# Optimization experiments

Hardware: AMD Instinct MI355X
Metric: run time of the kernel (lower is better)

## Reference

```python
import jax, jax.numpy as jnp
import numpy as np
from jax import lax


def ternarize(w):
    """Standard TWN ternarization with straight-through estimator.
    delta = 0.7*mean(|w|); alpha = mean(|w|) over kept entries; w_t = alpha*sign(w)*mask.
    """
    a = jnp.abs(w)
    delta = 0.7 * a.mean()
    mask = (a > delta).astype(w.dtype)
    alpha = (a * mask).sum() / jnp.maximum(mask.sum(), 1.0)
    wt = alpha * jnp.sign(w) * mask
    return w + lax.stop_gradient(wt - w)  # STE


def conv3x3(x, w, b):
    y = lax.conv_general_dilated(x, ternarize(w), window_strides=(1, 1),
                                 padding=((1, 1), (1, 1)),
                                 dimension_numbers=('NCHW', 'OIHW', 'NCHW'))
    return y + b[None, :, None, None]


def maxpool2(x):
    return lax.reduce_window(x, -jnp.inf, lax.max, (1, 1, 2, 2), (1, 1, 2, 2), 'VALID')


def setup_inputs() -> dict:
    key = jax.random.key(0)
    ks = jax.random.split(key, 11)
    s = lambda k, shape, scale: jax.random.normal(k, shape, dtype=jnp.float32) * scale
    return {
        'x':   s(ks[0], (1024, 3, 32, 32), 1.0),
        'w1':  s(ks[1], (64, 3, 3, 3), 0.1),
        'b1':  s(ks[2], (64,), 0.01),
        'w2':  s(ks[3], (128, 64, 3, 3), 0.05),
        'b2':  s(ks[4], (128,), 0.01),
        'w3':  s(ks[5], (256, 128, 3, 3), 0.03),
        'b3':  s(ks[6], (256,), 0.01),
        'wf1': s(ks[7], (256, 4096), 0.02),
        'bf1': s(ks[8], (256,), 0.01),
        'wf2': s(ks[9], (10, 256), 0.06),
        'bf2': s(ks[10], (10,), 0.01),
    }


def reference(x, w1, b1, w2, b2, w3, b3, wf1, bf1, wf2, bf2):
    x = maxpool2(jax.nn.relu(conv3x3(x, w1, b1)))   # [B,64,16,16]
    x = maxpool2(jax.nn.relu(conv3x3(x, w2, b2)))   # [B,128,8,8]
    x = maxpool2(jax.nn.relu(conv3x3(x, w3, b3)))   # [B,256,4,4]
    x = x.reshape(-1, 256 * 4 * 4)
    x = jax.nn.relu(x @ ternarize(wf1).T + bf1)     # [B,256]
    return x @ ternarize(wf2).T + bf2               # [B,10]
```

## Files before the change

kernel.cpp:

```cpp
#include <hip/hip_runtime.h>
#include <hip/hip_bf16.h>


typedef __attribute__((ext_vector_type(8))) short short8;
typedef __attribute__((ext_vector_type(4))) float f32x4;
typedef __attribute__((ext_vector_type(4))) int i32x4;

#define GLOAD_LDS16(g, l)                                              \
    __builtin_amdgcn_global_load_lds(                                  \
        (const __attribute__((address_space(1))) void*)(g),            \
        (__attribute__((address_space(3))) void*)(l), 16, 0, 0)

__device__ __forceinline__ unsigned short f2bf(float x) {
    unsigned u = __float_as_uint(x);
    return (unsigned short)((u + 0x7fffu + ((u >> 16) & 1u)) >> 16);
}
__device__ __forceinline__ float bf2f(unsigned short b) {
    return __uint_as_float(((unsigned)b) << 16);
}

#define WS_W1B   0
#define N_W1B    2048
#define WS_W2P   (WS_W1B + N_W1B)
#define N_W2P    (9*128*64)
#define WS_W3P   (WS_W2P + N_W2P)
#define N_W3P    (9*256*128)
#define WS_WTF1  (WS_W3P + N_W3P)
#define N_WTF1   (256*4096)
#define WS_WTF2  (WS_WTF1 + N_WTF1)
#define N_WTF2   (10*256)
#define WS_A1    (WS_WTF2 + N_WTF2)
#define N_A1     (1024*256*64)
#define WS_A2    (WS_A1 + N_A1)
#define N_A2     (1024*64*128)
#define WS_A3    (WS_A2 + N_A2)
#define N_A3     (1024*16*256)
#define WS_F1    (WS_A3 + N_A3)
#define N_F1     (1024*256)
#define WS_SCR   (WS_F1 + N_F1)

#define FC1_S    16

struct TernArgs {
    const float* w[6];
    int n[6];
};

__global__ void tern_stats1(TernArgs ta, double* __restrict__ scr) {
    const int wi = blockIdx.y;
    const float* __restrict__ w = ta.w[wi];
    const int n = ta.n[wi];
    __shared__ double red[4];
    const int lane = threadIdx.x & 63, wv = threadIdx.x >> 6;
    if (wi == 5) {
        float m = 0.f;
        for (int i = blockIdx.x * blockDim.x + threadIdx.x; i < n;
             i += gridDim.x * blockDim.x)
            m = fmaxf(m, fabsf(w[i]));
        #pragma unroll
        for (int off = 32; off > 0; off >>= 1)
            m = fmaxf(m, __shfl_down(m, off, 64));
        if (lane == 0) red[wv] = (double)m;
        __syncthreads();
        if (threadIdx.x == 0) {
            float mm = (float)fmax(fmax(red[0], red[1]), fmax(red[2], red[3]));
            atomicMax((int*)(scr + 20), __float_as_int(mm));
        }
        return;
    }
    double s = 0.0;
    for (int i = blockIdx.x * blockDim.x + threadIdx.x; i < n;
         i += gridDim.x * blockDim.x)
        s += (double)fabsf(w[i]);
    #pragma unroll
    for (int off = 32; off > 0; off >>= 1) s += __shfl_down(s, off, 64);
    if (lane == 0) red[wv] = s;
    __syncthreads();
    if (threadIdx.x == 0)
        atomicAdd(scr + wi * 4, red[0] + red[1] + red[2] + red[3]);
}

__global__ void tern_stats2(TernArgs ta, double* __restrict__ scr) {
    const int wi = blockIdx.y;
    const float* __restrict__ w = ta.w[wi];
    const int n = ta.n[wi];
    const float delta = (float)(0.7 * scr[wi * 4] / (double)n);
    double ms = 0.0, cnt = 0.0;
    for (int i = blockIdx.x * blockDim.x + threadIdx.x; i < n;
         i += gridDim.x * blockDim.x) {
        float a = fabsf(w[i]);
        if (a > delta) { ms += (double)a; cnt += 1.0; }
    }
    #pragma unroll
    for (int off = 32; off > 0; off >>= 1) {
        ms += __shfl_down(ms, off, 64);
        cnt += __shfl_down(cnt, off, 64);
    }
    __shared__ double redm[4], redc[4];
    const int lane = threadIdx.x & 63, wv = threadIdx.x >> 6;
    if (lane == 0) { redm[wv] = ms; redc[wv] = cnt; }
    __syncthreads();
    if (threadIdx.x == 0) {
        atomicAdd(scr + wi * 4 + 1, redm[0] + redm[1] + redm[2] + redm[3]);
        atomicAdd(scr + wi * 4 + 2, redc[0] + redc[1] + redc[2] + redc[3]);
    }
}

__global__ void tern_write_all(TernArgs ta, const double* __restrict__ scr,
                               signed char* __restrict__ w1b,
                               signed char* __restrict__ w2p8,
                               signed char* __restrict__ w3p8,
                               unsigned short* __restrict__ wtf1b,
                               float* __restrict__ wtf2) {
    const int wi = blockIdx.y;
    const float* __restrict__ w = ta.w[wi];
    const int n = ta.n[wi];
    const double* sc = scr + wi * 4;
    const float delta = (float)(0.7 * sc[0] / (double)n);
    const int i0 = blockIdx.x * blockDim.x + threadIdx.x;
    const int stride = gridDim.x * blockDim.x;

    if (wi == 0) {
        for (int i = i0; i < n; i += stride) {
            const int co = i / 27;
            const int kp = i % 27;
            float v = w[i];
            signed char s = (fabsf(v) > delta) ? (v > 0.0f ? 1 : -1) : 0;
            w1b[co * 64 + kp] = s;
            w1b[4096 + co * 64 + 32 + kp] = s;
        }
    } else if (wi == 4) {
        const double c = sc[2];
        const float alpha = (float)(sc[1] / (c > 1.0 ? c : 1.0));
        for (int i = i0; i < n; i += stride) {
            float v = w[i];
            wtf2[i] = (fabsf(v) > delta) ? (v > 0.0f ? alpha : -alpha) : 0.0f;
        }
    } else if (wi == 1 || wi == 2) {
        const int CIc = (wi == 1) ? 64 : 128;
        const int COc = (wi == 1) ? 128 : 256;
        signed char* dst = (wi == 1) ? w2p8 : w3p8;
        for (int i = i0; i < n; i += stride) {
            const int co = i / (CIc * 9);
            const int r = i % (CIc * 9);
            const int ci = r / 9, tap = r % 9;
            float v = w[i];
            signed char s = (fabsf(v) > delta) ? (v > 0.0f ? 1 : -1) : 0;
            dst[(tap * COc + co) * CIc + ci] = s;
        }
    } else {
        for (int i = i0; i < n; i += stride) {
            const int j = i >> 12;
            const int k = i & 4095;
            const int c = k >> 4, px = k & 15;
            float v = w[i];
            unsigned short s = (fabsf(v) > delta) ? (v > 0.0f ? 0x3f80 : 0xbf80) : 0;
            unsigned short* row = wtf1b + ((long)j << 13) + px * 512 + c;
            row[0] = s;
            row[256] = s;
        }
    }
}

__global__ __launch_bounds__(256) void conv1_i8(
        const float* __restrict__ x,
        const signed char* __restrict__ w1b,
        const float* __restrict__ bias,
        const double* __restrict__ scr,
        const int* __restrict__ amax_x,
        int* __restrict__ amax_out,
        float* __restrict__ y) {
    constexpr int PL = 3472;
    __shared__ __align__(16) char X[2 * PL];
    __shared__ float redm[4];

    const int b = blockIdx.x;
    const int tid = threadIdx.x;
    const float S = 32512.0f / fmaxf(__int_as_float(*amax_x), 1e-30f);

    for (int i = tid; i < 2 * PL / 16; i += 256)
        ((int4*)X)[i] = make_int4(0, 0, 0, 0);
    __syncthreads();

    for (int i = tid; i < 768; i += 256) {
        const float4 v = ((const float4*)(x + (long)b * 3072))[i];
        const int e = i * 4;
        const int ci = e >> 10;
        const int rem = e & 1023;
        const int h = rem >> 5, w = rem & 31;
        const int base = ci * 1156 + (h + 1) * 34 + (w + 1);
        const float f[4] = {v.x, v.y, v.z, v.w};
        #pragma unroll
        for (int j = 0; j < 4; j++) {
            const int q = __float2int_rn(f[j] * S);
            const int ql = (q << 24) >> 24;
            const int qh = (q - ql) >> 8;
            X[base + j] = (char)ql;
            X[PL + base + j] = (char)qh;
        }
    }
    __syncthreads();

    const int lane = tid & 63;
    const int wid = tid >> 6;
    const int lm = lane & 15;
    const int kg = lane >> 4;

    const int poff = (kg >= 2) ? PL : 0;
    int cst[16];
    #pragma unroll
    for (int j = 0; j < 16; j++) {
        const int kp = (kg & 1) * 16 + j;
        cst[j] = (kp < 27)
                     ? ((kp / 9) * 1156 + ((kp % 9) / 3) * 34 + (kp % 9) % 3)
                     : 0;
    }

    i32x4 BL[4], BH[4];
    #pragma unroll
    for (int nt = 0; nt < 4; nt++) {
        const int co = nt * 16 + lm;
        BL[nt] = *(const i32x4*)(w1b + (long)co * 64 + kg * 16);
        BH[nt] = *(const i32x4*)(w1b + 4096 + (long)co * 64 + kg * 16);
    }

    const double c2 = scr[2];
    const float alpha = (float)(scr[1] / (c2 > 1.0 ? c2 : 1.0));
    const float dq = alpha / S;
    float tmax = 0.f;
    float* yb = y + (long)b * 256 * 64;

    for (int tt = 0; tt < 16; ++tt) {
        const int t = wid * 16 + tt;
        const int pp = t * 4 + (lm >> 2);
        const int sub = lm & 3;
        const int h = 2 * (pp >> 4) + (sub >> 1);
        const int w = 2 * (pp & 15) + (sub & 1);
        const int base = poff + h * 34 + w;
        unsigned d[4] = {0u, 0u, 0u, 0u};
        #pragma unroll
        for (int j = 0; j < 16; j++) {
            const unsigned byte = (unsigned char)X[base + cst[j]];
            d[j >> 2] |= byte << ((j & 3) * 8);
        }
        i32x4 Af;
        Af[0] = (int)d[0]; Af[1] = (int)d[1];
        Af[2] = (int)d[2]; Af[3] = (int)d[3];

        const int opp = t * 4 + kg;
        float* yr = yb + (long)opp * 64;
        #pragma unroll
        for (int nt = 0; nt < 4; nt++) {
            i32x4 aL = 0, aH = 0;
            aL = __builtin_amdgcn_mfma_i32_16x16x64_i8(Af, BL[nt], aL, 0, 0, 0);
            aH = __builtin_amdgcn_mfma_i32_16x16x64_i8(Af, BH[nt], aH, 0, 0, 0);
            const int s0 = aH[0] * 256 + aL[0];
            const int s1 = aH[1] * 256 + aL[1];
            const int s2 = aH[2] * 256 + aL[2];
            const int s3 = aH[3] * 256 + aL[3];
            int sm = s0 > s1 ? s0 : s1;
            const int sn = s2 > s3 ? s2 : s3;
            sm = sm > sn ? sm : sn;
            const int co = nt * 16 + lm;
            const float o = fmaxf(dq * (float)sm + bias[co], 0.f);
            tmax = fmaxf(tmax, o);
            yr[co] = o;
        }
    }

    #pragma unroll
    for (int off = 32; off > 0; off >>= 1)
        tmax = fmaxf(tmax, __shfl_down(tmax, off, 64));
    if (lane == 0) redm[wid] = tmax;
    __syncthreads();
    if (tid == 0) {
        float m = fmaxf(fmaxf(redm[0], redm[1]), fmaxf(redm[2], redm[3]));
        atomicMax(amax_out, __float_as_int(m));
    }
}

template <int CI, int HI, int CO, int HB, int WM, int WN, bool INF32>
__global__ __launch_bounds__(256, 2) void conv_i8(
        const void* __restrict__ xin,
        const signed char* __restrict__ wp,
        const float* __restrict__ bias,
        const double* __restrict__ scr,
        const int* __restrict__ amax_in,
        int* __restrict__ amax_out,
        unsigned short* __restrict__ yout) {
    constexpr int CH8 = CI / 64;
    constexpr int NITER = 9 * CH8;
    constexpr int HR = HI / HB;
    constexpr int ROWS = HR + 2;
    constexpr int COLS = HI + 2;
    constexpr int NPIX = ROWS * COLS;
    constexpr int PSTR = NPIX * 64 + 32;
    constexpr int PO = HI / 2;
    constexpr int POR = HR / 2;
    constexpr int MT = 4, NT = 4;
    constexpr int RWB = HI * CI * 4;
    constexpr int RAWR = (HB == 1) ? (ROWS - 2) : (ROWS - 1);
    static_assert(WM * WN == 4, "4 waves");
    static_assert(WM * 64 == HR * HI, "M covers slab pixels");
    static_assert(WN * 64 == CO, "N covers all co");
    static_assert(RWB == 4096, "row must be 4096 B");
    static_assert(HB <= 2, "row compaction assumes <=1 invalid row per end");
    static_assert((COLS & 1) == 0, "swizzle parity uses even COLS");

    __shared__ __align__(16) char X[2 * CH8 * PSTR];
    __shared__ __align__(16) char RAW[RAWR * RWB];
    __shared__ float redm[4];

    const int bimg = blockIdx.x / HB;
    const int hb = blockIdx.x % HB;
    const int tid = threadIdx.x;
    const int lane = tid & 63;
    const int wid = tid >> 6;

    const float S = 32512.0f / fmaxf(__int_as_float(*amax_in), 1e-30f);

    const int rlo = (hb == 0) ? 1 : 0;
    const int rhi = (hb == HB - 1) ? (ROWS - 1) : ROWS;
    for (int r = rlo; r < rhi; r++) {
        if (wid == (r & 3)) {
            const int h = hb * HR + r - 1;
            const int rl = r - rlo;
            const char* grow = (const char*)xin +
                               ((long)(bimg * HI + h)) * RWB;
            #pragma unroll
            for (int j = 0; j < RWB / 1024; j++)
                GLOAD_LDS16(grow + j * 1024 + lane * 16,
                            &RAW[rl * RWB + j * 1024]);
        }
    }

    constexpr int HALO = 2 * COLS + 2 * (ROWS - 2);
    for (int i = tid; i < HALO * 2 * CH8 * 4; i += 256) {
        const int u = i & 3;
        const int t = i >> 2;
        const int g = t % (2 * CH8);
        const int hp = t / (2 * CH8);
        int p;
        if (hp < COLS) p = hp;
        else if (hp < 2 * COLS) p = (ROWS - 1) * COLS + (hp - COLS);
        else {
            const int e = hp - 2 * COLS;
            p = (1 + (e >> 1)) * COLS + ((e & 1) ? (COLS - 1) : 0);
        }
        *(int4*)&X[g * PSTR + p * 64 + u * 16] = make_int4(0, 0, 0, 0);
    }
    __syncthreads();

    if (INF32) {
        constexpr int NIT = RAWR * HI * (CI / 4);
        for (int i = tid; i < NIT; i += 256) {
            const int q4 = i % (CI / 4);
            const int t = i / (CI / 4);
            const int c = t % HI;
            const int rl = t / HI;
            const int r = rlo + rl;
            const float4 v =
                *(const float4*)&RAW[rl * RWB + c * (CI * 4) + q4 * 16];
            const float f[4] = {v.x, v.y, v.z, v.w};
            unsigned pl = 0, ph = 0;
            #pragma unroll
            for (int j = 0; j < 4; j++) {
                const int qi = (int)(f[j] * S + 0.5f);
                pl |= (unsigned)(qi & 255) << (j * 8);
                ph |= (unsigned)(((qi + 128) >> 8) & 255) << (j * 8);
            }
            const int p = r * COLS + c + 1;
            const int cc = (q4 * 4) & 63;
            const int ch = q4 / 16;
            const int slot = ((cc >> 4) + ((c + 1) >> 1) + 2 * r) & 3;
            const int base = p * 64 + slot * 16 + (cc & 15);
            *(unsigned*)&X[ch * PSTR + base] = pl;
            *(unsigned*)&X[(CH8 + ch) * PSTR + base] = ph;
        }
    } else {
        constexpr int NIT = RAWR * HI * (CI / 8);
        for (int i = tid; i < NIT; i += 256) {
            const int q8 = i % (CI / 8);
            const int t = i / (CI / 8);
            const int c = t % HI;
            const int rl = t / HI;
            const int r = rlo + rl;
            const uint4 vh =
                *(const uint4*)&RAW[rl * RWB + c * (CI * 4) + q8 * 16];
            const uint4 vl =
                *(const uint4*)&RAW[rl * RWB + c * (CI * 4) + CI * 2 +
                                    q8 * 16];
            const unsigned* hw = (const unsigned*)&vh;
            const unsigned* lw = (const unsigned*)&vl;
            float f[8];
            #pragma unroll
            for (int j = 0; j < 8; j++) {
                const unsigned hu = (j & 1) ? (hw[j >> 1] >> 16)
                                            : (hw[j >> 1] & 0xffffu);
                const unsigned lu = (j & 1) ? (lw[j >> 1] >> 16)
                                            : (lw[j >> 1] & 0xffffu);
                f[j] = __uint_as_float(hu << 16) + __uint_as_float(lu << 16);
            }
            unsigned pl0 = 0, pl1 = 0, ph0 = 0, ph1 = 0;
            #pragma unroll
            for (int j = 0; j < 8; j++) {
                const int qi = (int)(f[j] * S + 0.5f);
                const int sh = (j & 3) * 8;
                const unsigned lb = (unsigned)(qi & 255) << sh;
                const unsigned hbyte =
                    (unsigned)(((qi + 128) >> 8) & 255) << sh;
                if (j < 4) { pl0 |= lb; ph0 |= hbyte; }
                else       { pl1 |= lb; ph1 |= hbyte; }
            }
            const int p = r * COLS + c + 1;
            const int ch = q8 / 8;
            const int cc = (q8 * 8) & 63;
            const int slot = ((cc >> 4) + ((c + 1) >> 1) + 2 * r) & 3;
            const int base = p * 64 + slot * 16 + (cc & 15);
            *(uint2*)&X[ch * PSTR + base] = make_uint2(pl0, pl1);
            *(uint2*)&X[(CH8 + ch) * PSTR + base] = make_uint2(ph0, ph1);
        }
    }
    __syncthreads();

    const int wm = (WM == 1) ? 0 : (wid >> 1);
    const int wn = (WM == 1) ? wid : (wid & 1);
    const int lm = lane & 15;
    const int kg = lane >> 4;

    int pq[MT];
    #pragma unroll
    for (int mt = 0; mt < MT; mt++) {
        const int m = (wm * MT + mt) * 16 + lm;
        const int pp = m >> 2, sub = m & 3;
        const int lph = pp / PO, lpw = pp % PO;
        const int h = 2 * lph + (sub >> 1);
        const int w = 2 * lpw + (sub & 1);
        pq[mt] = ((h * COLS + w) << 6) | ((h & 1) << 3) | (w & 7);
    }
    const signed char* bp[NT];
    #pragma unroll
    for (int nt = 0; nt < NT; nt++) {
        const int co = (wn * NT + nt) * 16 + lm;
        bp[nt] = wp + (long)co * CI + kg * 16;
    }

    i32x4 accL[MT][NT], accH[MT][NT];
    #pragma unroll
    for (int mt = 0; mt < MT; mt++)
        #pragma unroll
        for (int nt = 0; nt < NT; nt++) { accL[mt][nt] = 0; accH[mt][nt] = 0; }

    i32x4 Bb[2][NT];
    #pragma unroll
    for (int nt = 0; nt < NT; nt++) Bb[0][nt] = *(const i32x4*)(bp[nt]);

    #pragma unroll 2
    for (int it = 0; it < NITER; ++it) {
        const int cur = it & 1, nxt = cur ^ 1;
        if (it + 1 < NITER) {
            const int it1 = it + 1;
            const int tap = it1 / CH8, ch1 = it1 % CH8;
            const int woff = tap * CO * CI + ch1 * 64;
            #pragma unroll
            for (int nt = 0; nt < NT; nt++)
                Bb[nxt][nt] = *(const i32x4*)(bp[nt] + woff);
        }
        const int tap = it / CH8, ch = it % CH8;
        const int ty = tap / 3, tx = tap % 3;
        const int DT = (ty * COLS + tx) << 6;
        const int typ = ty & 1;
        int ao[MT];
        #pragma unroll
        for (int mt = 0; mt < MT; mt++) {
            const int q = pq[mt];
            const int slot = (kg + ((((q >> 3) & 1) + typ) & 1) * 2 +
                              (((q & 7) + tx) >> 1)) & 3;
            ao[mt] = (q & ~63) + DT + (slot << 4);
        }
        {
            i32x4 Af[MT];
            #pragma unroll
            for (int mt = 0; mt < MT; mt++)
                Af[mt] = *(const i32x4*)&X[ch * PSTR + ao[mt]];
            #pragma unroll
            for (int mt = 0; mt < MT; mt++)
                #pragma unroll
                for (int nt = 0; nt < NT; nt++)
                    accL[mt][nt] = __builtin_amdgcn_mfma_i32_16x16x64_i8(
                        Af[mt], Bb[cur][nt], accL[mt][nt], 0, 0, 0);
        }
        {
            i32x4 Af[MT];
            #pragma unroll
            for (int mt = 0; mt < MT; mt++)
                Af[mt] = *(const i32x4*)&X[(CH8 + ch) * PSTR + ao[mt]];
            #pragma unroll
            for (int mt = 0; mt < MT; mt++)
                #pragma unroll
                for (int nt = 0; nt < NT; nt++)
                    accH[mt][nt] = __builtin_amdgcn_mfma_i32_16x16x64_i8(
                        Af[mt], Bb[cur][nt], accH[mt][nt], 0, 0, 0);
        }
    }

    const double c2 = scr[2];
    const float alpha = (float)(scr[1] / (c2 > 1.0 ? c2 : 1.0));
    const float dq = alpha / S;
    float tmax = 0.f;
    #pragma unroll
    for (int mt = 0; mt < MT; mt++) {
        const int pp = (wm * MT + mt) * 4 + kg;
        const int lph = pp / PO, lpw = pp % PO;
        const int gpp = (hb * POR + lph) * PO + lpw;
        unsigned short* yr = yout + ((long)bimg * (PO * PO) + gpp) * (2 * CO);
        #pragma unroll
        for (int nt = 0; nt < NT; nt++) {
            const int co = (wn * NT + nt) * 16 + lm;
            const i32x4 aL = accL[mt][nt], aH = accH[mt][nt];
            int s0 = aH[0] * 256 + aL[0];
            int s1 = aH[1] * 256 + aL[1];
            int s2 = aH[2] * 256 + aL[2];
            int s3 = aH[3] * 256 + aL[3];
            int sm = s0 > s1 ? s0 : s1;
            int sn = s2 > s3 ? s2 : s3;
            sm = sm > sn ? sm : sn;
            float o = fmaxf(dq * (float)sm + bias[co], 0.f);
            tmax = fmaxf(tmax, o);
            unsigned short hi = f2bf(o);
            unsigned short lo = f2bf(o - bf2f(hi));
            yr[co] = hi;
            yr[CO + co] = lo;
        }
    }
    if (amax_out) {
        #pragma unroll
        for (int off = 32; off > 0; off >>= 1)
            tmax = fmaxf(tmax, __shfl_down(tmax, off, 64));
        if (lane == 0) redm[wid] = tmax;
        __syncthreads();
        if (tid == 0) {
            float m = fmaxf(fmaxf(redm[0], redm[1]), fmaxf(redm[2], redm[3]));
            atomicMax(amax_out, __float_as_int(m));
        }
    }
}

template <int S>
__global__ __launch_bounds__(256) void fc1_mfma(
        const unsigned short* __restrict__ A,
        const unsigned short* __restrict__ Bw,
        float* __restrict__ parts) {
    constexpr int KCH = 8192 / S;
    constexpr int NSTEP = KCH / 32;
    const int m0 = blockIdx.x * 128;
    const int n0 = blockIdx.y * 128;
    const int s = blockIdx.z;
    const int tid = threadIdx.x;
    const int lane = tid & 63, wid = tid >> 6;
    const int wm = wid >> 1, wn = wid & 1;
    const int lm = lane & 15, kg = lane >> 4;

    const long k0 = (long)s * KCH + kg * 8;
    const unsigned short* ap[4];
    const unsigned short* bp[4];
    #pragma unroll
    for (int t = 0; t < 4; t++) {
        ap[t] = A + (long)(m0 + wm * 64 + t * 16 + lm) * 8192 + k0;
        bp[t] = Bw + (long)(n0 + wn * 64 + t * 16 + lm) * 8192 + k0;
    }

    f32x4 acc[4][4] = {};
    short8 Ab[2][4], Bb[2][4];
    #pragma unroll
    for (int t = 0; t < 4; t++) {
        Ab[0][t] = *(const short8*)(ap[t]);
        Bb[0][t] = *(const short8*)(bp[t]);
    }

    #pragma unroll 2
    for (int st = 0; st < NSTEP; ++st) {
        const int cur = st & 1, nxt = cur ^ 1;
        if (st + 1 < NSTEP) {
            const int off = (st + 1) * 32;
            #pragma unroll
            for (int t = 0; t < 4; t++) {
                Ab[nxt][t] = *(const short8*)(ap[t] + off);
                Bb[nxt][t] = *(const short8*)(bp[t] + off);
            }
        }
        #pragma unroll
        for (int mt = 0; mt < 4; mt++)
            #pragma unroll
            for (int nt = 0; nt < 4; nt++)
                acc[mt][nt] = __builtin_amdgcn_mfma_f32_16x16x32_bf16(
                    Ab[cur][mt], Bb[cur][nt], acc[mt][nt], 0, 0, 0);
    }

    #pragma unroll
    for (int mt = 0; mt < 4; mt++) {
        #pragma unroll
        for (int r = 0; r < 4; r++) {
            const int b = m0 + wm * 64 + mt * 16 + kg * 4 + r;
            #pragma unroll
            for (int nt = 0; nt < 4; nt++) {
                const int j = n0 + wn * 64 + nt * 16 + lm;
                parts[((long)s * 1024 + b) * 256 + j] = acc[mt][nt][r];
            }
        }
    }
}

template <int S>
__global__ __launch_bounds__(256) void fc2_fused(
        const float* __restrict__ parts,
        const double* __restrict__ scr,
        const float* __restrict__ bf1v,
        const float* __restrict__ wtf2,
        const float* __restrict__ bf2v,
        float* __restrict__ out) {
    __shared__ float sf[256];
    const int b = blockIdx.x;
    const int j = threadIdx.x;
    float s = 0.f;
    #pragma unroll
    for (int p = 0; p < S; p++)
        s += parts[(long)p * 262144 + (long)b * 256 + j];
    const double c2 = scr[2];
    const float alpha = (float)(scr[1] / (c2 > 1.0 ? c2 : 1.0));
    sf[j] = fmaxf(alpha * s + bf1v[j], 0.f);
    __syncthreads();
    const int lane = threadIdx.x & 63, wid = threadIdx.x >> 6;
    for (int k = wid; k < 10; k += 4) {
        const float* wr = wtf2 + k * 256;
        float acc = 0.f;
        #pragma unroll
        for (int t = 0; t < 4; t++)
            acc += sf[lane + t * 64] * wr[lane + t * 64];
        #pragma unroll
        for (int off = 32; off > 0; off >>= 1)
            acc += __shfl_down(acc, off, 64);
        if (lane == 0) out[(long)b * 10 + k] = acc + bf2v[k];
    }
}

extern "C" void kernel_launch(void* const* d_in, const int* in_sizes, int n_in,
                              void* d_out, int out_size, void* d_ws, size_t ws_size,
                              hipStream_t stream) {
    const float* x   = (const float*)d_in[0];
    const float* w1  = (const float*)d_in[1];
    const float* b1  = (const float*)d_in[2];
    const float* w2  = (const float*)d_in[3];
    const float* b2  = (const float*)d_in[4];
    const float* w3  = (const float*)d_in[5];
    const float* b3  = (const float*)d_in[6];
    const float* wf1 = (const float*)d_in[7];
    const float* bf1 = (const float*)d_in[8];
    const float* wf2 = (const float*)d_in[9];
    const float* bf2 = (const float*)d_in[10];
    float* out = (float*)d_out;
    float* ws = (float*)d_ws;

    const int B = 1024;

    signed char*    w1b   = (signed char*)(ws + WS_W1B);
    signed char*    w2p8  = (signed char*)(ws + WS_W2P);
    signed char*    w3p8  = (signed char*)(ws + WS_W3P);
    unsigned short* wtf1b = (unsigned short*)(ws + WS_WTF1);
    float*          wtf2  = ws + WS_WTF2;
    float*          a1f   = ws + WS_A1;
    unsigned short* a2p   = (unsigned short*)(ws + WS_A2);
    unsigned short* a3p   = (unsigned short*)(ws + WS_A3);
    double*         scr   = (double*)(ws + WS_SCR);
    int*            iscr  = (int*)(scr + 20);
    int*            amaxx = iscr;
    int*            amax1 = iscr + 1;
    int*            amax2 = iscr + 2;
    float*          parts = ws + WS_A1;

    hipMemsetAsync(scr, 0, 22 * sizeof(double), stream);
    hipMemsetAsync(w1b, 0, 8192, stream);

    TernArgs ta;
    ta.w[0] = w1;  ta.n[0] = 64 * 27;
    ta.w[1] = w2;  ta.n[1] = 128 * 64 * 9;
    ta.w[2] = w3;  ta.n[2] = 256 * 128 * 9;
    ta.w[3] = wf1; ta.n[3] = 256 * 4096;
    ta.w[4] = wf2; ta.n[4] = 10 * 256;
    ta.w[5] = x;   ta.n[5] = 1024 * 3 * 32 * 32;

    hipLaunchKernelGGL(tern_stats1, dim3(128, 6), dim3(256), 0, stream, ta, scr);
    hipLaunchKernelGGL(tern_stats2, dim3(128, 5), dim3(256), 0, stream, ta, scr);
    hipLaunchKernelGGL(tern_write_all, dim3(128, 5), dim3(256), 0, stream,
                       ta, scr, w1b, w2p8, w3p8, wtf1b, wtf2);

    hipLaunchKernelGGL(conv1_i8, dim3(B), dim3(256), 0, stream,
                       x, w1b, b1, scr + 0, amaxx, amax1, a1f);

    hipLaunchKernelGGL((conv_i8<64, 16, 128, 2, 2, 2, true>), dim3(B * 2),
                       dim3(256), 0, stream, a1f, w2p8, b2, scr + 4, amax1,
                       amax2, a2p);

    hipLaunchKernelGGL((conv_i8<128, 8, 256, 1, 1, 4, false>), dim3(B),
                       dim3(256), 0, stream, a2p, w3p8, b3, scr + 8, amax2,
                       (int*)nullptr, a3p);

    hipLaunchKernelGGL((fc1_mfma<FC1_S>), dim3(8, 2, FC1_S), dim3(256), 0, stream,
                       a3p, wtf1b, parts);

    hipLaunchKernelGGL((fc2_fused<FC1_S>), dim3(B), dim3(256), 0, stream,
                       parts, scr + 12, bf1, wtf2, bf2, out);
}
```

Baseline: 280.6 us.

## Process multiple slabs per block and prefetch next slab during epilogue

The conv_i8 kernel becomes persistent over NSLAB slabs per block, halving the grid for conv2 and conv3. The next slab's raw rows are issued via global_load_lds before the current slab's epilogue stores, overlapping load latency with output writes, and bias is hoisted into registers. Halo zeroing runs only once, except for the bottom row, which is re-zeroed when slabs alternate. The trade is fewer blocks, so less parallelism and occupancy across CUs, in exchange for amortized setup and overlapped loads.

```diff
diff --git a/kernel.cpp b/kernel.cpp
--- a/kernel.cpp
+++ b/kernel.cpp
@@ -279,7 +279,7 @@
     }
 }
 
-template <int CI, int HI, int CO, int HB, int WM, int WN, bool INF32>
+template <int CI, int HI, int CO, int HB, int WM, int WN, bool INF32, int NSLAB>
 __global__ __launch_bounds__(256, 2) void conv_i8(
         const void* __restrict__ xin,
         const signed char* __restrict__ wp,
@@ -311,117 +311,14 @@
     __shared__ __align__(16) char RAW[RAWR * RWB];
     __shared__ float redm[4];
 
-    const int bimg = blockIdx.x / HB;
-    const int hb = blockIdx.x % HB;
     const int tid = threadIdx.x;
     const int lane = tid & 63;
     const int wid = tid >> 6;
 
     const float S = 32512.0f / fmaxf(__int_as_float(*amax_in), 1e-30f);
-
-    const int rlo = (hb == 0) ? 1 : 0;
-    const int rhi = (hb == HB - 1) ? (ROWS - 1) : ROWS;
-    for (int r = rlo; r < rhi; r++) {
-        if (wid == (r & 3)) {
-            const int h = hb * HR + r - 1;
-            const int rl = r - rlo;
-            const char* grow = (const char*)xin +
-                               ((long)(bimg * HI + h)) * RWB;
-            #pragma unroll
-            for (int j = 0; j < RWB / 1024; j++)
-                GLOAD_LDS16(grow + j * 1024 + lane * 16,
-                            &RAW[rl * RWB + j * 1024]);
-        }
-    }
-
-    constexpr int HALO = 2 * COLS + 2 * (ROWS - 2);
-    for (int i = tid; i < HALO * 2 * CH8 * 4; i += 256) {
-        const int u = i & 3;
-        const int t = i >> 2;
-        const int g = t % (2 * CH8);
-        const int hp = t / (2 * CH8);
-        int p;
-        if (hp < COLS) p = hp;
-        else if (hp < 2 * COLS) p = (ROWS - 1) * COLS + (hp - COLS);
-        else {
-            const int e = hp - 2 * COLS;
-            p = (1 + (e >> 1)) * COLS + ((e & 1) ? (COLS - 1) : 0);
-        }
-        *(int4*)&X[g * PSTR + p * 64 + u * 16] = make_int4(0, 0, 0, 0);
-    }
-    __syncthreads();
-
-    if (INF32) {
-        constexpr int NIT = RAWR * HI * (CI / 4);
-        for (int i = tid; i < NIT; i += 256) {
-            const int q4 = i % (CI / 4);
-            const int t = i / (CI / 4);
-            const int c = t % HI;
-            const int rl = t / HI;
-            const int r = rlo + rl;
-            const float4 v =
-                *(const float4*)&RAW[rl * RWB + c * (CI * 4) + q4 * 16];
-            const float f[4] = {v.x, v.y, v.z, v.w};
-            unsigned pl = 0, ph = 0;
-            #pragma unroll
-            for (int j = 0; j < 4; j++) {
-                const int qi = (int)(f[j] * S + 0.5f);
-                pl |= (unsigned)(qi & 255) << (j * 8);
-                ph |= (unsigned)(((qi + 128) >> 8) & 255) << (j * 8);
-            }
-            const int p = r * COLS + c + 1;
-            const int cc = (q4 * 4) & 63;
-            const int ch = q4 / 16;
-            const int slot = ((cc >> 4) + ((c + 1) >> 1) + 2 * r) & 3;
-            const int base = p * 64 + slot * 16 + (cc & 15);
-            *(unsigned*)&X[ch * PSTR + base] = pl;
-            *(unsigned*)&X[(CH8 + ch) * PSTR + base] = ph;
-        }
-    } else {
-        constexpr int NIT = RAWR * HI * (CI / 8);
-        for (int i = tid; i < NIT; i += 256) {
-            const int q8 = i % (CI / 8);
-            const int t = i / (CI / 8);
-            const int c = t % HI;
-            const int rl = t / HI;
-            const int r = rlo + rl;
-            const uint4 vh =
-                *(const uint4*)&RAW[rl * RWB + c * (CI * 4) + q8 * 16];
-            const uint4 vl =
-                *(const uint4*)&RAW[rl * RWB + c * (CI * 4) + CI * 2 +
-                                    q8 * 16];
-            const unsigned* hw = (const unsigned*)&vh;
-            const unsigned* lw = (const unsigned*)&vl;
-            float f[8];
-            #pragma unroll
-            for (int j = 0; j < 8; j++) {
-                const unsigned hu = (j & 1) ? (hw[j >> 1] >> 16)
-                                            : (hw[j >> 1] & 0xffffu);
-                const unsigned lu = (j & 1) ? (lw[j >> 1] >> 16)
-                                            : (lw[j >> 1] & 0xffffu);
-                f[j] = __uint_as_float(hu << 16) + __uint_as_float(lu << 16);
-            }
-            unsigned pl0 = 0, pl1 = 0, ph0 = 0, ph1 = 0;
-            #pragma unroll
-            for (int j = 0; j < 8; j++) {
-                const int qi = (int)(f[j] * S + 0.5f);
-                const int sh = (j & 3) * 8;
-                const unsigned lb = (unsigned)(qi & 255) << sh;
-                const unsigned hbyte =
-                    (unsigned)(((qi + 128) >> 8) & 255) << sh;
-                if (j < 4) { pl0 |= lb; ph0 |= hbyte; }
-                else       { pl1 |= lb; ph1 |= hbyte; }
-            }
-            const int p = r * COLS + c + 1;
-            const int ch = q8 / 8;
-            const int cc = (q8 * 8) & 63;
-            const int slot = ((cc >> 4) + ((c + 1) >> 1) + 2 * r) & 3;
-            const int base = p * 64 + slot * 16 + (cc & 15);
-            *(uint2*)&X[ch * PSTR + base] = make_uint2(pl0, pl1);
-            *(uint2*)&X[(CH8 + ch) * PSTR + base] = make_uint2(ph0, ph1);
-        }
-    }
-    __syncthreads();
+    const double c2 = scr[2];
+    const float alpha = (float)(scr[1] / (c2 > 1.0 ? c2 : 1.0));
+    const float dq = alpha / S;
 
     const int wm = (WM == 1) ? 0 : (wid >> 1);
     const int wn = (WM == 1) ? wid : (wid & 1);
@@ -439,100 +336,249 @@
         pq[mt] = ((h * COLS + w) << 6) | ((h & 1) << 3) | (w & 7);
     }
     const signed char* bp[NT];
+    float bias_r[NT];
     #pragma unroll
     for (int nt = 0; nt < NT; nt++) {
         const int co = (wn * NT + nt) * 16 + lm;
         bp[nt] = wp + (long)co * CI + kg * 16;
-    }
-
-    i32x4 accL[MT][NT], accH[MT][NT];
-    #pragma unroll
-    for (int mt = 0; mt < MT; mt++)
-        #pragma unroll
-        for (int nt = 0; nt < NT; nt++) { accL[mt][nt] = 0; accH[mt][nt] = 0; }
-
-    i32x4 Bb[2][NT];
-    #pragma unroll
-    for (int nt = 0; nt < NT; nt++) Bb[0][nt] = *(const i32x4*)(bp[nt]);
-
-    #pragma unroll 2
-    for (int it = 0; it < NITER; ++it) {
-        const int cur = it & 1, nxt = cur ^ 1;
-        if (it + 1 < NITER) {
-            const int it1 = it + 1;
-            const int tap = it1 / CH8, ch1 = it1 % CH8;
-            const int woff = tap * CO * CI + ch1 * 64;
+        bias_r[nt] = bias[co];
+    }
+
+    float tmax = 0.f;
+
+    for (int s = 0; s < NSLAB; ++s) {
+        const int gs = blockIdx.x * NSLAB + s;
+        const int bimg = gs / HB;
+        const int hb = gs % HB;
+        const int rlo = (hb == 0) ? 1 : 0;
+        const int rhi = (hb == HB - 1) ? (ROWS - 1) : ROWS;
+
+        if (s == 0) {
+            for (int r = rlo; r < rhi; r++) {
+                if (wid == (r & 3)) {
+                    const int h = hb * HR + r - 1;
+                    const int rl = r - rlo;
+                    const char* grow = (const char*)xin +
+                                       ((long)(bimg * HI + h)) * RWB;
+                    #pragma unroll
+                    for (int j = 0; j < RWB / 1024; j++)
+                        GLOAD_LDS16(grow + j * 1024 + lane * 16,
+                                    &RAW[rl * RWB + j * 1024]);
+                }
+            }
+            constexpr int HALO = 2 * COLS + 2 * (ROWS - 2);
+            for (int i = tid; i < HALO * 2 * CH8 * 4; i += 256) {
+                const int u = i & 3;
+                const int t = i >> 2;
+                const int g = t % (2 * CH8);
+                const int hp = t / (2 * CH8);
+                int p;
+                if (hp < COLS) p = hp;
+                else if (hp < 2 * COLS) p = (ROWS - 1) * COLS + (hp - COLS);
+                else {
+                    const int e = hp - 2 * COLS;
+                    p = (1 + (e >> 1)) * COLS + ((e & 1) ? (COLS - 1) : 0);
+                }
+                *(int4*)&X[g * PSTR + p * 64 + u * 16] = make_int4(0, 0, 0, 0);
+            }
+            __syncthreads();
+        }
+
+        i32x4 Bb[2][NT];
+        #pragma unroll
+        for (int nt = 0; nt < NT; nt++) Bb[0][nt] = *(const i32x4*)(bp[nt]);
+
+        if (HB > 1 && s > 0) {
+            for (int i = tid; i < (COLS - 2) * 2 * CH8 * 4; i += 256) {
+                const int u = i & 3;
+                const int t = i >> 2;
+                const int g = t % (2 * CH8);
+                const int cc = t / (2 * CH8);
+                const int p = (ROWS - 1) * COLS + 1 + cc;
+                *(int4*)&X[g * PSTR + p * 64 + u * 16] = make_int4(0, 0, 0, 0);
+            }
+        }
+
+        if (INF32) {
+            constexpr int NIT = RAWR * HI * (CI / 4);
+            for (int i = tid; i < NIT; i += 256) {
+                const int q4 = i % (CI / 4);
+                const int t = i / (CI / 4);
+                const int c = t % HI;
+                const int rl = t / HI;
+                const int r = rlo + rl;
+                const float4 v =
+                    *(const float4*)&RAW[rl * RWB + c * (CI * 4) + q4 * 16];
+                const float f[4] = {v.x, v.y, v.z, v.w};
+                unsigned pl = 0, ph = 0;
+                #pragma unroll
+                for (int j = 0; j < 4; j++) {
+                    const int qi = (int)(f[j] * S + 0.5f);
+                    pl |= (unsigned)(qi & 255) << (j * 8);
+                    ph |= (unsigned)(((qi + 128) >> 8) & 255) << (j * 8);
+                }
+                const int p = r * COLS + c + 1;
+                const int cc = (q4 * 4) & 63;
+                const int ch = q4 / 16;
+                const int slot = ((cc >> 4) + ((c + 1) >> 1) + 2 * r) & 3;
+                const int base = p * 64 + slot * 16 + (cc & 15);
+                *(unsigned*)&X[ch * PSTR + base] = pl;
+                *(unsigned*)&X[(CH8 + ch) * PSTR + base] = ph;
+            }
+        } else {
+            constexpr int NIT = RAWR * HI * (CI / 8);
+            for (int i = tid; i < NIT; i += 256) {
+                const int q8 = i % (CI / 8);
+                const int t = i / (CI / 8);
+                const int c = t % HI;
+                const int rl = t / HI;
+                const int r = rlo + rl;
+                const uint4 vh =
+                    *(const uint4*)&RAW[rl * RWB + c * (CI * 4) + q8 * 16];
+                const uint4 vl =
+                    *(const uint4*)&RAW[rl * RWB + c * (CI * 4) + CI * 2 +
+                                        q8 * 16];
+                const unsigned* hw = (const unsigned*)&vh;
+                const unsigned* lw = (const unsigned*)&vl;
+                float f[8];
+                #pragma unroll
+                for (int j = 0; j < 8; j++) {
+                    const unsigned hu = (j & 1) ? (hw[j >> 1] >> 16)
+                                                : (hw[j >> 1] & 0xffffu);
+                    const unsigned lu = (j & 1) ? (lw[j >> 1] >> 16)
+                                                : (lw[j >> 1] & 0xffffu);
+                    f[j] = __uint_as_float(hu << 16) +
+                           __uint_as_float(lu << 16);
+                }
+                unsigned pl0 = 0, pl1 = 0, ph0 = 0, ph1 = 0;
+                #pragma unroll
+                for (int j = 0; j < 8; j++) {
+                    const int qi = (int)(f[j] * S + 0.5f);
+                    const int sh = (j & 3) * 8;
+                    const unsigned lb = (unsigned)(qi & 255) << sh;
+                    const unsigned hbyte =
+                        (unsigned)(((qi + 128) >> 8) & 255) << sh;
+                    if (j < 4) { pl0 |= lb; ph0 |= hbyte; }
+                    else       { pl1 |= lb; ph1 |= hbyte; }
+                }
+                const int p = r * COLS + c + 1;
+                const int ch = q8 / 8;
+                const int cc = (q8 * 8) & 63;
+                const int slot = ((cc >> 4) + ((c + 1) >> 1) + 2 * r) & 3;
+                const int base = p * 64 + slot * 16 + (cc & 15);
+                *(uint2*)&X[ch * PSTR + base] = make_uint2(pl0, pl1);
+                *(uint2*)&X[(CH8 + ch) * PSTR + base] = make_uint2(ph0, ph1);
+            }
+        }
+        __syncthreads();
+
+        i32x4 accL[MT][NT], accH[MT][NT];
+        #pragma unroll
+        for (int mt = 0; mt < MT; mt++)
             #pragma unroll
-            for (int nt = 0; nt < NT; nt++)
-                Bb[nxt][nt] = *(const i32x4*)(bp[nt] + woff);
-        }
-        const int tap = it / CH8, ch = it % CH8;
-        const int ty = tap / 3, tx = tap % 3;
-        const int DT = (ty * COLS + tx) << 6;
-        const int typ = ty & 1;
-        int ao[MT];
-        #pragma unroll
-        for (int mt = 0; mt < MT; mt++) {
-            const int q = pq[mt];
-            const int slot = (kg + ((((q >> 3) & 1) + typ) & 1) * 2 +
-                              (((q & 7) + tx) >> 1)) & 3;
-            ao[mt] = (q & ~63) + DT + (slot << 4);
-        }
-        {
-            i32x4 Af[MT];
-            #pragma unroll
-            for (int mt = 0; mt < MT; mt++)
-                Af[mt] = *(const i32x4*)&X[ch * PSTR + ao[mt]];
-            #pragma unroll
-            for (int mt = 0; mt < MT; mt++)
+            for (int nt = 0; nt < NT; nt++) {
+                accL[mt][nt] = 0; accH[mt][nt] = 0;
+            }
+
+        #pragma unroll 2
+        for (int it = 0; it < NITER; ++it) {
+            const int cur = it & 1, nxt = cur ^ 1;
+            if (it + 1 < NITER) {
+                const int it1 = it + 1;
+                const int tap = it1 / CH8, ch1 = it1 % CH8;
+                const int woff = tap * CO * CI + ch1 * 64;
                 #pragma unroll
                 for (int nt = 0; nt < NT; nt++)
-                    accL[mt][nt] = __builtin_amdgcn_mfma_i32_16x16x64_i8(
-                        Af[mt], Bb[cur][nt], accL[mt][nt], 0, 0, 0);
-        }
-        {
-            i32x4 Af[MT];
+                    Bb[nxt][nt] = *(const i32x4*)(bp[nt] + woff);
+            }
+            const int tap = it / CH8, ch = it % CH8;
+            const int ty = tap / 3, tx = tap % 3;
+            const int DT = (ty * COLS + tx) << 6;
+            const int typ = ty & 1;
+            int ao[MT];
             #pragma unroll
-            for (int mt = 0; mt < MT; mt++)
-                Af[mt] = *(const i32x4*)&X[(CH8 + ch) * PSTR + ao[mt]];
+            for (int mt = 0; mt < MT; mt++) {
+                const int q = pq[mt];
+                const int slot = (kg + ((((q >> 3) & 1) + typ) & 1) * 2 +
+                                  (((q & 7) + tx) >> 1)) & 3;
+                ao[mt] = (q & ~63) + DT + (slot << 4);
+            }
+            {
+                i32x4 Af[MT];
+                #pragma unroll
+                for (int mt = 0; mt < MT; mt++)
+                    Af[mt] = *(const i32x4*)&X[ch * PSTR + ao[mt]];
+                #pragma unroll
+                for (int mt = 0; mt < MT; mt++)
+                    #pragma unroll
+                    for (int nt = 0; nt < NT; nt++)
+                        accL[mt][nt] = __builtin_amdgcn_mfma_i32_16x16x64_i8(
+                            Af[mt], Bb[cur][nt], accL[mt][nt], 0, 0, 0);
+            }
+            {
+                i32x4 Af[MT];
+                #pragma unroll
+                for (int mt = 0; mt < MT; mt++)
+                    Af[mt] = *(const i32x4*)&X[(CH8 + ch) * PSTR + ao[mt]];
+                #pragma unroll
+                for (int mt = 0; mt < MT; mt++)
+                    #pragma unroll
+                    for (int nt = 0; nt < NT; nt++)
+                        accH[mt][nt] = __builtin_amdgcn_mfma_i32_16x16x64_i8(
+                            Af[mt], Bb[cur][nt], accH[mt][nt], 0, 0, 0);
+            }
+        }
+
+        if (s + 1 < NSLAB) {
+            const int gs1 = gs + 1;
+            const int bimg1 = gs1 / HB;
+            const int hb1 = gs1 % HB;
+            const int rlo1 = (hb1 == 0) ? 1 : 0;
+            const int rhi1 = (hb1 == HB - 1) ? (ROWS - 1) : ROWS;
+            for (int r = rlo1; r < rhi1; r++) {
+                if (wid == (r & 3)) {
+                    const int h = hb1 * HR + r - 1;
+                    const int rl = r - rlo1;
+                    const char* grow = (const char*)xin +
+                                       ((long)(bimg1 * HI + h)) * RWB;
+                    #pragma unroll
+                    for (int j = 0; j < RWB / 1024; j++)
+                        GLOAD_LDS16(grow + j * 1024 + lane * 16,
+                                    &RAW[rl * RWB + j * 1024]);
+                }
+            }
+        }
+
+        #pragma unroll
+        for (int mt = 0; mt < MT; mt++) {
+            const int pp = (wm * MT + mt) * 4 + kg;
+            const int lph = pp / PO, lpw = pp % PO;
+            const int gpp = (hb * POR + lph) * PO + lpw;
+            unsigned short* yr =
+                yout + ((long)bimg * (PO * PO) + gpp) * (2 * CO);
             #pragma unroll
-            for (int mt = 0; mt < MT; mt++)
-                #pragma unroll
-                for (int nt = 0; nt < NT; nt++)
-                    accH[mt][nt] = __builtin_amdgcn_mfma_i32_16x16x64_i8(
-                        Af[mt], Bb[cur][nt], accH[mt][nt], 0, 0, 0);
-        }
-    }
-
-    const double c2 = scr[2];
-    const float alpha = (float)(scr[1] / (c2 > 1.0 ? c2 : 1.0));
-    const float dq = alpha / S;
-    float tmax = 0.f;
-    #pragma unroll
-    for (int mt = 0; mt < MT; mt++) {
-        const int pp = (wm * MT + mt) * 4 + kg;
-        const int lph = pp / PO, lpw = pp % PO;
-        const int gpp = (hb * POR + lph) * PO + lpw;
-        unsigned short* yr = yout + ((long)bimg * (PO * PO) + gpp) * (2 * CO);
-        #pragma unroll
-        for (int nt = 0; nt < NT; nt++) {
-            const int co = (wn * NT + nt) * 16 + lm;
-            const i32x4 aL = accL[mt][nt], aH = accH[mt][nt];
-            int s0 = aH[0] * 256 + aL[0];
-            int s1 = aH[1] * 256 + aL[1];
-            int s2 = aH[2] * 256 + aL[2];
-            int s3 = aH[3] * 256 + aL[3];
-            int sm = s0 > s1 ? s0 : s1;
-            int sn = s2 > s3 ? s2 : s3;
-            sm = sm > sn ? sm : sn;
-            float o = fmaxf(dq * (float)sm + bias[co], 0.f);
-            tmax = fmaxf(tmax, o);
-            unsigned short hi = f2bf(o);
-            unsigned short lo = f2bf(o - bf2f(hi));
-            yr[co] = hi;
-            yr[CO + co] = lo;
-        }
-    }
+            for (int nt = 0; nt < NT; nt++) {
+                const int co = (wn * NT + nt) * 16 + lm;
+                const i32x4 aL = accL[mt][nt], aH = accH[mt][nt];
+                int s0 = aH[0] * 256 + aL[0];
+                int s1 = aH[1] * 256 + aL[1];
+                int s2 = aH[2] * 256 + aL[2];
+                int s3 = aH[3] * 256 + aL[3];
+                int sm = s0 > s1 ? s0 : s1;
+                int sn = s2 > s3 ? s2 : s3;
+                sm = sm > sn ? sm : sn;
+                float o = fmaxf(dq * (float)sm + bias_r[nt], 0.f);
+                tmax = fmaxf(tmax, o);
+                unsigned short hi = f2bf(o);
+                unsigned short lo = f2bf(o - bf2f(hi));
+                yr[co] = hi;
+                yr[CO + co] = lo;
+            }
+        }
+
+        if (s + 1 < NSLAB) __syncthreads();
+    }
+
     if (amax_out) {
         #pragma unroll
         for (int off = 32; off > 0; off >>= 1)
@@ -697,11 +743,11 @@
     hipLaunchKernelGGL(conv1_i8, dim3(B), dim3(256), 0, stream,
                        x, w1b, b1, scr + 0, amaxx, amax1, a1f);
 
-    hipLaunchKernelGGL((conv_i8<64, 16, 128, 2, 2, 2, true>), dim3(B * 2),
+    hipLaunchKernelGGL((conv_i8<64, 16, 128, 2, 2, 2, true, 2>), dim3(B),
                        dim3(256), 0, stream, a1f, w2p8, b2, scr + 4, amax1,
                        amax2, a2p);
 
-    hipLaunchKernelGGL((conv_i8<128, 8, 256, 1, 1, 4, false>), dim3(B),
+    hipLaunchKernelGGL((conv_i8<128, 8, 256, 1, 1, 4, false, 2>), dim3(B / 2),
                        dim3(256), 0, stream, a2p, w3p8, b3, scr + 8, amax2,
                        (int*)nullptr, a3p);
 
```

New measurement: 338.4 us. 20.6% more time.

## Quantize conv1 output to int8 planes using analytic bound, feed conv2 directly

Applied to the files above, without the earlier changes.

Conv1 no longer writes float activations and computes a runtime amax. It now derives a static upper bound on its output scale from alpha1, the maximum per-channel nonzero count, amax(x) and max|bias|, and writes pre-swizzled int8 lo/hi planes. Conv2 gains a PREQ path that loads those planes straight into LDS, skipping the fp32 staging and in-kernel quantization, which cuts a1 traffic about 4x. The cost is a coarser, looser quantization scale for conv1 outputs, a tiny extra kernel, and FC1 split-K doubled to 32.

```diff
diff --git a/kernel.cpp b/kernel.cpp
--- a/kernel.cpp
+++ b/kernel.cpp
@@ -17,6 +17,14 @@
 }
 __device__ __forceinline__ float bf2f(unsigned short b) {
     return __uint_as_float(((unsigned)b) << 16);
+}
+
+__device__ __forceinline__ float calc_S1(const double* __restrict__ scr,
+                                         float amaxx) {
+    const double c2 = scr[2];
+    const float alpha1 = (float)(scr[1] / (c2 > 1.0 ? c2 : 1.0));
+    const float ub = alpha1 * (float)scr[22] * amaxx + (float)scr[23];
+    return 32512.0f / fmaxf(ub, 1e-30f);
 }
 
 #define WS_W1B   0
@@ -39,7 +47,7 @@
 #define N_F1     (1024*256)
 #define WS_SCR   (WS_F1 + N_F1)
 
-#define FC1_S    16
+#define FC1_S    32
 
 struct TernArgs {
     const float* w[6];
@@ -104,6 +112,24 @@
         atomicAdd(scr + wi * 4 + 1, redm[0] + redm[1] + redm[2] + redm[3]);
         atomicAdd(scr + wi * 4 + 2, redc[0] + redc[1] + redc[2] + redc[3]);
     }
+}
+
+__global__ void nnz_pass(const float* __restrict__ w1,
+                         const float* __restrict__ b1,
+                         double* __restrict__ scr) {
+    const float delta = (float)(0.7 * scr[0] / 1728.0);
+    const int t = threadIdx.x;
+    int cnt = 0;
+    #pragma unroll
+    for (int k = 0; k < 27; k++)
+        cnt += (fabsf(w1[t * 27 + k]) > delta) ? 1 : 0;
+    float bb = fabsf(b1[t]);
+    #pragma unroll
+    for (int off = 32; off > 0; off >>= 1) {
+        cnt = max(cnt, __shfl_down(cnt, off, 64));
+        bb = fmaxf(bb, __shfl_down(bb, off, 64));
+    }
+    if (t == 0) { scr[22] = (double)cnt; scr[23] = (double)bb; }
 }
 
 __global__ void tern_write_all(TernArgs ta, const double* __restrict__ scr,
@@ -168,15 +194,15 @@
         const float* __restrict__ bias,
         const double* __restrict__ scr,
         const int* __restrict__ amax_x,
-        int* __restrict__ amax_out,
-        float* __restrict__ y) {
+        signed char* __restrict__ a1q) {
     constexpr int PL = 3472;
     __shared__ __align__(16) char X[2 * PL];
-    __shared__ float redm[4];
 
     const int b = blockIdx.x;
     const int tid = threadIdx.x;
-    const float S = 32512.0f / fmaxf(__int_as_float(*amax_x), 1e-30f);
+    const float amx = fmaxf(__int_as_float(*amax_x), 1e-30f);
+    const float S = 32512.0f / amx;
+    const float S1 = calc_S1(scr, __int_as_float(*amax_x));
 
     for (int i = tid; i < 2 * PL / 16; i += 256)
         ((int4*)X)[i] = make_int4(0, 0, 0, 0);
@@ -227,8 +253,7 @@
     const double c2 = scr[2];
     const float alpha = (float)(scr[1] / (c2 > 1.0 ? c2 : 1.0));
     const float dq = alpha / S;
-    float tmax = 0.f;
-    float* yb = y + (long)b * 256 * 64;
+    signed char* yb = a1q + (long)b * 32768;
 
     for (int tt = 0; tt < 16; ++tt) {
         const int t = wid * 16 + tt;
@@ -248,7 +273,8 @@
         Af[2] = (int)d[2]; Af[3] = (int)d[3];
 
         const int opp = t * 4 + kg;
-        float* yr = yb + (long)opp * 64;
+        const int ho = opp >> 4, wo = opp & 15;
+        signed char* yrow = yb + ((long)ho * 2048) + wo * 64;
         #pragma unroll
         for (int nt = 0; nt < 4; nt++) {
             i32x4 aL = 0, aH = 0;
@@ -263,23 +289,18 @@
             sm = sm > sn ? sm : sn;
             const int co = nt * 16 + lm;
             const float o = fmaxf(dq * (float)sm + bias[co], 0.f);
-            tmax = fmaxf(tmax, o);
-            yr[co] = o;
-        }
-    }
-
-    #pragma unroll
-    for (int off = 32; off > 0; off >>= 1)
-        tmax = fmaxf(tmax, __shfl_down(tmax, off, 64));
-    if (lane == 0) redm[wid] = tmax;
-    __syncthreads();
-    if (tid == 0) {
-        float m = fmaxf(fmaxf(redm[0], redm[1]), fmaxf(redm[2], redm[3]));
-        atomicMax(amax_out, __float_as_int(m));
-    }
-}
-
-template <int CI, int HI, int CO, int HB, int WM, int WN, bool INF32>
+            const int q = (int)(o * S1 + 0.5f);
+            const int ql = (q << 24) >> 24;
+            const int qh = (q + 128) >> 8;
+            const int slot = (nt + ((wo + 1) >> 1) + 2 * (ho + 1)) & 3;
+            const int off = slot * 16 + lm;
+            yrow[off] = (char)ql;
+            yrow[1024 + off] = (char)qh;
+        }
+    }
+}
+
+template <int CI, int HI, int CO, int HB, int WM, int WN, bool PREQ, int WIDX>
 __global__ __launch_bounds__(256, 2) void conv_i8(
         const void* __restrict__ xin,
         const signed char* __restrict__ wp,
@@ -299,16 +320,18 @@
     constexpr int POR = HR / 2;
     constexpr int MT = 4, NT = 4;
     constexpr int RWB = HI * CI * 4;
-    constexpr int RAWR = (HB == 1) ? (ROWS - 2) : (ROWS - 1);
+    constexpr int RWQ = HI * 64 * 2;
+    constexpr int RAWR = PREQ ? 1 : ((HB == 1) ? (ROWS - 2) : (ROWS - 1));
     static_assert(WM * WN == 4, "4 waves");
     static_assert(WM * 64 == HR * HI, "M covers slab pixels");
     static_assert(WN * 64 == CO, "N covers all co");
-    static_assert(RWB == 4096, "row must be 4096 B");
+    static_assert(PREQ || RWB == 4096, "row must be 4096 B");
+    static_assert(!PREQ || CH8 == 1, "PREQ path assumes CI==64");
     static_assert(HB <= 2, "row compaction assumes <=1 invalid row per end");
     static_assert((COLS & 1) == 0, "swizzle parity uses even COLS");
 
     __shared__ __align__(16) char X[2 * CH8 * PSTR];
-    __shared__ __align__(16) char RAW[RAWR * RWB];
+    __shared__ __align__(16) char RAW[PREQ ? 16 : RAWR * RWB];
     __shared__ float redm[4];
 
     const int bimg = blockIdx.x / HB;
@@ -317,67 +340,80 @@
     const int lane = tid & 63;
     const int wid = tid >> 6;
 
-    const float S = 32512.0f / fmaxf(__int_as_float(*amax_in), 1e-30f);
+    float S;
+    if (PREQ) S = calc_S1(scr, __int_as_float(*amax_in));
+    else      S = 32512.0f / fmaxf(__int_as_float(*amax_in), 1e-30f);
 
     const int rlo = (hb == 0) ? 1 : 0;
     const int rhi = (hb == HB - 1) ? (ROWS - 1) : ROWS;
-    for (int r = rlo; r < rhi; r++) {
-        if (wid == (r & 3)) {
-            const int h = hb * HR + r - 1;
-            const int rl = r - rlo;
-            const char* grow = (const char*)xin +
-                               ((long)(bimg * HI + h)) * RWB;
-            #pragma unroll
-            for (int j = 0; j < RWB / 1024; j++)
-                GLOAD_LDS16(grow + j * 1024 + lane * 16,
-                            &RAW[rl * RWB + j * 1024]);
-        }
-    }
-
-    constexpr int HALO = 2 * COLS + 2 * (ROWS - 2);
-    for (int i = tid; i < HALO * 2 * CH8 * 4; i += 256) {
-        const int u = i & 3;
-        const int t = i >> 2;
-        const int g = t % (2 * CH8);
-        const int hp = t / (2 * CH8);
-        int p;
-        if (hp < COLS) p = hp;
-        else if (hp < 2 * COLS) p = (ROWS - 1) * COLS + (hp - COLS);
-        else {
-            const int e = hp - 2 * COLS;
-            p = (1 + (e >> 1)) * COLS + ((e & 1) ? (COLS - 1) : 0);
-        }
-        *(int4*)&X[g * PSTR + p * 64 + u * 16] = make_int4(0, 0, 0, 0);
-    }
-    __syncthreads();
-
-    if (INF32) {
-        constexpr int NIT = RAWR * HI * (CI / 4);
-        for (int i = tid; i < NIT; i += 256) {
-            const int q4 = i % (CI / 4);
-            const int t = i / (CI / 4);
-            const int c = t % HI;
-            const int rl = t / HI;
-            const int r = rlo + rl;
-            const float4 v =
-                *(const float4*)&RAW[rl * RWB + c * (CI * 4) + q4 * 16];
-            const float f[4] = {v.x, v.y, v.z, v.w};
-            unsigned pl = 0, ph = 0;
-            #pragma unroll
-            for (int j = 0; j < 4; j++) {
-                const int qi = (int)(f[j] * S + 0.5f);
-                pl |= (unsigned)(qi & 255) << (j * 8);
-                ph |= (unsigned)(((qi + 128) >> 8) & 255) << (j * 8);
+
+    if (PREQ) {
+        for (int r = rlo; r < rhi; r++) {
+            #pragma unroll
+            for (int pl = 0; pl < 2; pl++) {
+                if (wid == ((r * 2 + pl) & 3)) {
+                    const int h = hb * HR + r - 1;
+                    const char* src = (const char*)xin +
+                        (long)(bimg * HI + h) * RWQ + pl * (RWQ / 2) +
+                        lane * 16;
+                    GLOAD_LDS16(src, &X[pl * PSTR + (r * COLS + 1) * 64]);
+                }
             }
-            const int p = r * COLS + c + 1;
-            const int cc = (q4 * 4) & 63;
-            const int ch = q4 / 16;
-            const int slot = ((cc >> 4) + ((c + 1) >> 1) + 2 * r) & 3;
-            const int base = p * 64 + slot * 16 + (cc & 15);
-            *(unsigned*)&X[ch * PSTR + base] = pl;
-            *(unsigned*)&X[(CH8 + ch) * PSTR + base] = ph;
+        }
+        const int nfull = ((hb == 0) ? 1 : 0) + ((hb == HB - 1) ? 1 : 0);
+        const int NP1 = ROWS * 2;
+        const int NPZ = NP1 + nfull * (COLS - 2);
+        for (int i = tid; i < NPZ * 2 * 4; i += 256) {
+            const int u = i & 3;
+            const int t = i >> 2;
+            const int g = t % 2;
+            const int e = t / 2;
+            int p;
+            if (e < NP1) {
+                const int row = e >> 1;
+                p = row * COLS + ((e & 1) ? (COLS - 1) : 0);
+            } else {
+                const int e2 = e - NP1;
+                const int inFirst = (hb == 0) && (e2 < COLS - 2);
+                const int fr = inFirst ? 0 : (ROWS - 1);
+                const int cc = inFirst ? e2
+                                       : (e2 - ((hb == 0) ? (COLS - 2) : 0));
+                p = fr * COLS + 1 + cc;
+            }
+            *(int4*)&X[g * PSTR + p * 64 + u * 16] = make_int4(0, 0, 0, 0);
         }
     } else {
+        for (int r = rlo; r < rhi; r++) {
+            if (wid == (r & 3)) {
+                const int h = hb * HR + r - 1;
+                const int rl = r - rlo;
+                const char* grow = (const char*)xin +
+                                   ((long)(bimg * HI + h)) * RWB;
+                #pragma unroll
+                for (int j = 0; j < RWB / 1024; j++)
+                    GLOAD_LDS16(grow + j * 1024 + lane * 16,
+                                &RAW[rl * RWB + j * 1024]);
+            }
+        }
+        constexpr int HALO = 2 * COLS + 2 * (ROWS - 2);
+        for (int i = tid; i < HALO * 2 * CH8 * 4; i += 256) {
+            const int u = i & 3;
+            const int t = i >> 2;
+            const int g = t % (2 * CH8);
+            const int hp = t / (2 * CH8);
+            int p;
+            if (hp < COLS) p = hp;
+            else if (hp < 2 * COLS) p = (ROWS - 1) * COLS + (hp - COLS);
+            else {
+                const int e = hp - 2 * COLS;
+                p = (1 + (e >> 1)) * COLS + ((e & 1) ? (COLS - 1) : 0);
+            }
+            *(int4*)&X[g * PSTR + p * 64 + u * 16] = make_int4(0, 0, 0, 0);
+        }
+    }
+
+    if (!PREQ) {
+        __syncthreads();
         constexpr int NIT = RAWR * HI * (CI / 8);
         for (int i = tid; i < NIT; i += 256) {
             const int q8 = i % (CI / 8);
@@ -504,8 +540,9 @@
         }
     }
 
-    const double c2 = scr[2];
-    const float alpha = (float)(scr[1] / (c2 > 1.0 ? c2 : 1.0));
+    const double* wst = scr + WIDX * 4;
+    const double c2 = wst[2];
+    const float alpha = (float)(wst[1] / (c2 > 1.0 ? c2 : 1.0));
     const float dq = alpha / S;
     float tmax = 0.f;
     #pragma unroll
@@ -668,17 +705,16 @@
     signed char*    w3p8  = (signed char*)(ws + WS_W3P);
     unsigned short* wtf1b = (unsigned short*)(ws + WS_WTF1);
     float*          wtf2  = ws + WS_WTF2;
-    float*          a1f   = ws + WS_A1;
+    signed char*    a1q   = (signed char*)(ws + WS_A1);
     unsigned short* a2p   = (unsigned short*)(ws + WS_A2);
     unsigned short* a3p   = (unsigned short*)(ws + WS_A3);
     double*         scr   = (double*)(ws + WS_SCR);
     int*            iscr  = (int*)(scr + 20);
     int*            amaxx = iscr;
-    int*            amax1 = iscr + 1;
     int*            amax2 = iscr + 2;
     float*          parts = ws + WS_A1;
 
-    hipMemsetAsync(scr, 0, 22 * sizeof(double), stream);
+    hipMemsetAsync(scr, 0, 24 * sizeof(double), stream);
     hipMemsetAsync(w1b, 0, 8192, stream);
 
     TernArgs ta;
@@ -691,18 +727,19 @@
 
     hipLaunchKernelGGL(tern_stats1, dim3(128, 6), dim3(256), 0, stream, ta, scr);
     hipLaunchKernelGGL(tern_stats2, dim3(128, 5), dim3(256), 0, stream, ta, scr);
+    hipLaunchKernelGGL(nnz_pass, dim3(1), dim3(64), 0, stream, w1, b1, scr);
     hipLaunchKernelGGL(tern_write_all, dim3(128, 5), dim3(256), 0, stream,
                        ta, scr, w1b, w2p8, w3p8, wtf1b, wtf2);
 
     hipLaunchKernelGGL(conv1_i8, dim3(B), dim3(256), 0, stream,
-                       x, w1b, b1, scr + 0, amaxx, amax1, a1f);
-
-    hipLaunchKernelGGL((conv_i8<64, 16, 128, 2, 2, 2, true>), dim3(B * 2),
-                       dim3(256), 0, stream, a1f, w2p8, b2, scr + 4, amax1,
+                       x, w1b, b1, scr, amaxx, a1q);
+
+    hipLaunchKernelGGL((conv_i8<64, 16, 128, 2, 2, 2, true, 1>), dim3(B * 2),
+                       dim3(256), 0, stream, a1q, w2p8, b2, scr, amaxx,
                        amax2, a2p);
 
-    hipLaunchKernelGGL((conv_i8<128, 8, 256, 1, 1, 4, false>), dim3(B),
-                       dim3(256), 0, stream, a2p, w3p8, b3, scr + 8, amax2,
+    hipLaunchKernelGGL((conv_i8<128, 8, 256, 1, 1, 4, false, 2>), dim3(B),
+                       dim3(256), 0, stream, a2p, w3p8, b3, scr, amax2,
                        (int*)nullptr, a3p);
 
     hipLaunchKernelGGL((fc1_mfma<FC1_S>), dim3(8, 2, FC1_S), dim3(256), 0, stream,
```

Measured after the change: 284.1 us. About the same (+1.2%).
